# Performance work log

Hardware: AMD Instinct MI355X
Metric: run time of the kernel (lower is better)

The kernel has to match this reference:

```python
import jax, jax.numpy as jnp
import numpy as np

N_HEAD = 16

def setup_inputs() -> dict:
    key = jax.random.key(0)
    ks = jax.random.split(key, 5)
    C = 1024
    s = 0.02
    return {
        "x": jax.random.normal(ks[0], (4, 2048, C), dtype=jnp.float32),
        "w_attn": jax.random.normal(ks[1], (C, 3 * C), dtype=jnp.float32) * s,
        "b_attn": jnp.zeros((3 * C,), dtype=jnp.float32),
        "w_proj": jax.random.normal(ks[2], (C, C), dtype=jnp.float32) * s,
        "b_proj": jnp.zeros((C,), dtype=jnp.float32),
    }

def reference(x, w_attn, b_attn, w_proj, b_proj):
    B, T, C = x.shape
    H = N_HEAD
    D = C // H
    qkv = x @ w_attn + b_attn                      # [B,T,3C]
    q, k, v = jnp.split(qkv, 3, axis=-1)
    # [B,H,T,D]
    q = q.reshape(B, T, H, D).transpose(0, 2, 1, 3)
    k = k.reshape(B, T, H, D).transpose(0, 2, 1, 3)
    v = v.reshape(B, T, H, D).transpose(0, 2, 1, 3)
    scale = 1.0 / np.sqrt(D).astype(np.float32)
    attn = jnp.einsum('bhtd,bhsd->bhts', q, k) * scale   # [B,H,T,T]
    causal = jnp.tril(jnp.ones((T, T), dtype=bool))
    attn = jnp.where(causal, attn, -jnp.inf)
    attn = jax.nn.softmax(attn, axis=-1)
    y = jnp.einsum('bhts,bhsd->bhtd', attn, v)           # [B,H,T,D]
    y = y.transpose(0, 2, 1, 3).reshape(B, T, C)
    return y @ w_proj + b_proj
```

## Files before the change

kernel.cpp:

```cpp
#include <hip/hip_runtime.h>
#include <hip/hip_bf16.h>

typedef short short8 __attribute__((ext_vector_type(8)));
typedef float f32x4 __attribute__((ext_vector_type(4)));
typedef float f32x16 __attribute__((ext_vector_type(16)));

typedef __attribute__((address_space(1))) void as1_void;
typedef __attribute__((address_space(3))) void as3_void;

__device__ __forceinline__ unsigned short f2bf(float f) {
    __hip_bfloat16 h = __float2bfloat16(f);
    return __builtin_bit_cast(unsigned short, h);
}

__device__ __forceinline__ float exp2fast(float x) {
    return __builtin_amdgcn_exp2f(x);
}

__device__ __forceinline__ unsigned int cvtpk(float lo, float hi) {
    unsigned int r;
    asm("v_cvt_pk_bf16_f32 %0, %1, %2" : "=v"(r) : "v"(lo), "v"(hi));
    return r;
}

__device__ __forceinline__ void plswap(unsigned int& a, unsigned int& b) {
    asm("v_permlane32_swap_b32 %0, %1" : "+v"(a), "+v"(b));
}

__device__ __forceinline__ void gload16(const unsigned short* g, unsigned short* l) {
    __builtin_amdgcn_global_load_lds((as1_void*)g, (as3_void*)l, 16, 0, 0);
}

__global__ __launch_bounds__(256) void conv_f32_to_bf16(
    const float* __restrict__ in, unsigned short* __restrict__ out, int n4) {
    int i = blockIdx.x * 256 + threadIdx.x;
    if (i >= n4) return;
    float4 v = ((const float4*)in)[i];
    ushort4 o;
    o.x = f2bf(v.x); o.y = f2bf(v.y); o.z = f2bf(v.z); o.w = f2bf(v.w);
    ((ushort4*)out)[i] = o;
}

__global__ __launch_bounds__(256) void transpose2_f32_to_bf16(
    const float* __restrict__ Wa, const float* __restrict__ Wp,
    unsigned short* __restrict__ WTa, unsigned short* __restrict__ WTp) {
    __shared__ float tile[32][33];
    const int K = 1024;
    int bx = blockIdx.x;
    const float* W;
    unsigned short* WT;
    int N, n0;
    if (bx < 96) { W = Wa; WT = WTa; N = 3072; n0 = bx * 32; }
    else         { W = Wp; WT = WTp; N = 1024; n0 = (bx - 96) * 32; }
    int tx = threadIdx.x, ty = threadIdx.y;
    int k0 = blockIdx.y * 32;
#pragma unroll
    for (int j = 0; j < 4; ++j)
        tile[ty + j * 8][tx] = W[(size_t)(k0 + ty + j * 8) * N + n0 + tx];
    __syncthreads();
#pragma unroll
    for (int j = 0; j < 4; ++j)
        WT[(size_t)(n0 + ty + j * 8) * K + k0 + tx] = f2bf(tile[tx][ty + j * 8]);
}

template <int MODE>
__global__ __launch_bounds__(256, 2) void gemm_bt(
    const unsigned short* __restrict__ A,
    const unsigned short* __restrict__ Bt,
    const float* __restrict__ bias,
    void* __restrict__ out0,
    unsigned short* __restrict__ out1,
    int M, int N, int K) {
    __shared__ unsigned short sA[128 * 64];
    __shared__ unsigned short sB[128 * 64];
    const int tid = threadIdx.x;
    const int lane = tid & 63;
    const int w = tid >> 6;
    const int wr = (w >> 1) * 64;
    const int wc = (w & 1) * 64;
    const size_t arow0 = (size_t)blockIdx.x * 128;
    const size_t brow0 = (size_t)blockIdx.y * 128;

    const int grow = (w << 5) + (lane >> 3);
    const int gcolswz = (((lane & 7) ^ ((lane >> 3) & 7)) << 3);
    const unsigned short* pA0 = A + (arow0 + grow) * (size_t)K + gcolswz;
    const unsigned short* pB0 = Bt + (brow0 + grow) * (size_t)K + gcolswz;
    unsigned short* lA = sA + (w << 11);
    unsigned short* lB = sB + (w << 11);

    f32x4 acc[4][4] = {};
    const int fr = lane & 15;
    const int g = lane >> 4;

    for (int k0 = 0; k0 < K; k0 += 64) {
        __syncthreads();
#pragma unroll
        for (int j = 0; j < 4; ++j) {
            gload16(pA0 + (size_t)(j * 8) * K + k0, lA + j * 512);
            gload16(pB0 + (size_t)(j * 8) * K + k0, lB + j * 512);
        }
        __syncthreads();

#pragma unroll
        for (int kc = 0; kc < 2; ++kc) {
            short8 af[4], bfr[4];
#pragma unroll
            for (int i = 0; i < 4; ++i) {
                const int row = wr + i * 16 + fr;
                af[i] = *(const short8*)&sA[row * 64 +
                                            (((kc * 4 + g) ^ (row & 7)) << 3)];
            }
#pragma unroll
            for (int i = 0; i < 4; ++i) {
                const int row = wc + i * 16 + fr;
                bfr[i] = *(const short8*)&sB[row * 64 +
                                             (((kc * 4 + g) ^ (row & 7)) << 3)];
            }
#pragma unroll
            for (int mi = 0; mi < 4; ++mi)
#pragma unroll
                for (int ni = 0; ni < 4; ++ni)
                    acc[mi][ni] = __builtin_amdgcn_mfma_f32_16x16x32_bf16(
                        af[mi], bfr[ni], acc[mi][ni], 0, 0, 0);
        }
    }

    const int fq = (lane >> 4) << 2;
    if constexpr (MODE == 0) {
#pragma unroll
        for (int mi = 0; mi < 4; ++mi)
#pragma unroll
            for (int ni = 0; ni < 4; ++ni) {
                size_t r = arow0 + wr + mi * 16 + fq;
                size_t c = brow0 + wc + ni * 16 + fr;
                float bv = bias[c];
#pragma unroll
                for (int j = 0; j < 4; ++j)
                    ((float*)out0)[(r + j) * (size_t)N + c] = acc[mi][ni][j] + bv;
            }
    } else {
        const bool isv = (int)(brow0 + wc) >= 2048;
        if (isv) {
#pragma unroll
            for (int mi = 0; mi < 4; ++mi)
#pragma unroll
                for (int ni = 0; ni < 4; ++ni) {
                    int c = (int)brow0 + wc + ni * 16 + fr;
                    float bv = bias[c];
                    int cv = c - 2048;
                    int r0 = (int)arow0 + wr + mi * 16 + fq;
                    int bb = r0 >> 11, t0 = r0 & 2047;
                    unsigned int lo = (unsigned int)f2bf(acc[mi][ni][0] + bv) |
                                      ((unsigned int)f2bf(acc[mi][ni][1] + bv) << 16);
                    unsigned int hi = (unsigned int)f2bf(acc[mi][ni][2] + bv) |
                                      ((unsigned int)f2bf(acc[mi][ni][3] + bv) << 16);
                    *(uint2*)&out1[(((size_t)(bb * 1024 + cv)) << 11) + t0] =
                        make_uint2(lo, hi);
                }
        } else {
            const float qs = ((int)(brow0 + wc) < 1024) ? 0.125f * 1.4426950408889634f
                                                        : 1.0f;
#pragma unroll
            for (int mi = 0; mi < 4; ++mi)
#pragma unroll
                for (int ni = 0; ni < 4; ++ni) {
                    size_t r = arow0 + wr + mi * 16 + fq;
                    size_t c = brow0 + wc + ni * 16 + fr;
                    float bv = bias[c];
#pragma unroll
                    for (int j = 0; j < 4; ++j)
                        ((unsigned short*)out0)[(r + j) * 2048 + c] =
                            f2bf((acc[mi][ni][j] + bv) * qs);
                }
        }
    }
}

__global__ __launch_bounds__(256, 3) void attn_mfma(
    const unsigned short* __restrict__ qk,
    const unsigned short* __restrict__ vt,
    unsigned short* __restrict__ y,
    int BH) {
    constexpr int T = 2048;
    constexpr float THR = 8.0f;

    __shared__ __align__(16) unsigned short sK[2][64 * 64];
    __shared__ __align__(16) unsigned short sV[2][64 * 64];

    const int tid = threadIdx.x;
    const int lane = tid & 63;
    const int w = tid >> 6;
    const int l31 = lane & 31;
    const int b5 = lane >> 5;

    const int bh = blockIdx.x % BH;
    const int qt = 15 - blockIdx.x / BH;
    const int b = bh >> 4;
    const int h = bh & 15;
    const int q0 = qt << 7;
    const int qw0 = q0 + w * 32;

    const unsigned short* kbase = qk + ((size_t)(b * T)) * 2048 + 1024 + h * 64;
    const unsigned short* vbase = vt + ((size_t)(b * 1024 + h * 64)) * 2048;

    const int srow = tid >> 3;
    const int c16 = tid & 7;
    const int swz = ((c16 ^ (srow & 7)) << 3);

    short8 vones;
#pragma unroll
    for (int i = 0; i < 8; ++i) vones[i] = (short)0x3F80;

    short8 aq[4];
    {
        const unsigned short* qbase =
            qk + ((size_t)(b * T + qw0 + l31)) * 2048 + h * 64;
#pragma unroll
        for (int kc = 0; kc < 4; ++kc)
            aq[kc] = *(const short8*)(qbase + b5 * 8 + kc * 16);
    }

    f32x16 O0 = {}, O1 = {};
    f32x16 l_st = {};
    float m_st = -1e30f;

    const int nt = (q0 + 128) >> 6;

    uint4 kA0, kA1, kB0, kB1, vd0, vd1;
    kA0 = *(const uint4*)(kbase + (size_t)(srow) * 2048 + c16 * 8);
    kA1 = *(const uint4*)(kbase + (size_t)(srow + 32) * 2048 + c16 * 8);
    vd0 = *(const uint4*)(vbase + (size_t)srow * 2048 + c16 * 8);
    vd1 = *(const uint4*)(vbase + (size_t)(srow + 32) * 2048 + c16 * 8);
    *(uint4*)&sK[0][srow * 64 + swz] = kA0;
    *(uint4*)&sK[0][(srow + 32) * 64 + swz] = kA1;
    *(uint4*)&sV[0][srow * 64 + swz] = vd0;
    *(uint4*)&sV[0][(srow + 32) * 64 + swz] = vd1;
    kB0 = *(const uint4*)(kbase + (size_t)(64 + srow) * 2048 + c16 * 8);
    kB1 = *(const uint4*)(kbase + (size_t)(64 + srow + 32) * 2048 + c16 * 8);
    __syncthreads();

    for (int it = 0; it < nt; ++it) {
        const int s0 = it << 6;
        const bool haveNext = (it + 1 < nt);
        const bool have2 = (it + 2 < nt);
        if (it & 1) {
            if (have2) {
                const int s2 = s0 + 128;
                kB0 = *(const uint4*)(kbase + (size_t)(s2 + srow) * 2048 + c16 * 8);
                kB1 = *(const uint4*)(kbase + (size_t)(s2 + srow + 32) * 2048 +
                                      c16 * 8);
            }
        } else {
            if (have2) {
                const int s2 = s0 + 128;
                kA0 = *(const uint4*)(kbase + (size_t)(s2 + srow) * 2048 + c16 * 8);
                kA1 = *(const uint4*)(kbase + (size_t)(s2 + srow + 32) * 2048 +
                                      c16 * 8);
            }
        }
        if (haveNext) {
            const int s1 = s0 + 64;
            vd0 = *(const uint4*)(vbase + (size_t)srow * 2048 + s1 + c16 * 8);
            vd1 = *(const uint4*)(vbase + (size_t)(srow + 32) * 2048 + s1 + c16 * 8);
        }
        const unsigned short* sKc = sK[it & 1];
        const unsigned short* sVc = sV[it & 1];

        if (s0 <= qw0 + 31) {
            f32x16 sacc[2] = {};
            __builtin_amdgcn_s_setprio(1);
#pragma unroll
            for (int kc = 0; kc < 4; ++kc) {
#pragma unroll
                for (int ni = 0; ni < 2; ++ni) {
                    const int row = ni * 32 + l31;
                    short8 akf = *(const short8*)&sKc[row * 64 +
                                                      (((b5 + kc * 2) ^ (row & 7))
                                                       << 3)];
                    sacc[ni] = __builtin_amdgcn_mfma_f32_32x32x16_bf16(
                        akf, aq[kc], sacc[ni], 0, 0, 0);
                }
            }
            __builtin_amdgcn_s_setprio(0);

            const bool needMask = (s0 + 63 > qw0);
            const int qg = qw0 + l31;
            if (needMask) {
#pragma unroll
                for (int ni = 0; ni < 2; ++ni)
#pragma unroll
                    for (int reg = 0; reg < 16; ++reg) {
                        const int sg = s0 + ni * 32 + (reg & 3) + 8 * (reg >> 2) +
                                       4 * b5;
                        sacc[ni][reg] = (sg <= qg) ? sacc[ni][reg] : -INFINITY;
                    }
            }

            float mt[16];
#pragma unroll
            for (int i = 0; i < 16; ++i)
                mt[i] = fmaxf(sacc[0][i], sacc[1][i]);
#pragma unroll
            for (int st = 8; st > 0; st >>= 1)
#pragma unroll
                for (int i = 0; i < 8; ++i)
                    if (i < st) mt[i] = fmaxf(mt[i], mt[i + st]);
            float mx = mt[0];
            mx = fmaxf(mx, __shfl_xor(mx, 32));

            const bool resc = __any(mx > m_st + THR);
            float f_l = 1.0f;
            if (resc) {
                const float mn = fmaxf(m_st, mx);
                f_l = exp2fast(m_st - mn);
                m_st = mn;
            }

#pragma unroll
            for (int ni = 0; ni < 2; ++ni)
#pragma unroll
                for (int reg = 0; reg < 16; ++reg)
                    sacc[ni][reg] = exp2fast(sacc[ni][reg] - m_st);

            short8 pa[4];
#pragma unroll
            for (int c = 0; c < 4; ++c) {
                const int ni = c >> 1;
                const int off = (c & 1) * 8;
                unsigned int pk01 = cvtpk(sacc[ni][off + 0], sacc[ni][off + 1]);
                unsigned int pk23 = cvtpk(sacc[ni][off + 2], sacc[ni][off + 3]);
                unsigned int pk45 = cvtpk(sacc[ni][off + 4], sacc[ni][off + 5]);
                unsigned int pk67 = cvtpk(sacc[ni][off + 6], sacc[ni][off + 7]);
                plswap(pk01, pk45);
                plswap(pk23, pk67);
                uint4 u = make_uint4(pk01, pk23, pk45, pk67);
                pa[c] = __builtin_bit_cast(short8, u);
            }

            if (resc) {
                const int fil = __builtin_bit_cast(int, f_l);
#pragma unroll
                for (int reg = 0; reg < 16; ++reg) {
                    const int qpat = (reg & 3) + 8 * (reg >> 2) + 4 * b5;
                    const float fq = __builtin_bit_cast(
                        float, __builtin_amdgcn_ds_bpermute(
                                   (qpat + (lane & 32)) << 2, fil));
                    O0[reg] *= fq;
                    O1[reg] *= fq;
                    l_st[reg] *= fq;
                }
            }

            __builtin_amdgcn_s_setprio(1);
#pragma unroll
            for (int c = 0; c < 4; ++c) {
                l_st = __builtin_amdgcn_mfma_f32_32x32x16_bf16(
                    pa[c], vones, l_st, 0, 0, 0);
                {
                    const int row = l31;
                    short8 bvf = *(const short8*)&sVc[row * 64 +
                                                      (((c * 2 + b5) ^ (row & 7))
                                                       << 3)];
                    O0 = __builtin_amdgcn_mfma_f32_32x32x16_bf16(
                        pa[c], bvf, O0, 0, 0, 0);
                }
                {
                    const int row = 32 + l31;
                    short8 bvf = *(const short8*)&sVc[row * 64 +
                                                      (((c * 2 + b5) ^ (row & 7))
                                                       << 3)];
                    O1 = __builtin_amdgcn_mfma_f32_32x32x16_bf16(
                        pa[c], bvf, O1, 0, 0, 0);
                }
            }
            __builtin_amdgcn_s_setprio(0);
        }

        if (haveNext) {
            unsigned short* sKn = sK[(it + 1) & 1];
            unsigned short* sVn = sV[(it + 1) & 1];
            if (it & 1) {
                *(uint4*)&sKn[srow * 64 + swz] = kA0;
                *(uint4*)&sKn[(srow + 32) * 64 + swz] = kA1;
            } else {
                *(uint4*)&sKn[srow * 64 + swz] = kB0;
                *(uint4*)&sKn[(srow + 32) * 64 + swz] = kB1;
            }
            *(uint4*)&sVn[srow * 64 + swz] = vd0;
            *(uint4*)&sVn[(srow + 32) * 64 + swz] = vd1;
        }
        __syncthreads();
    }

#pragma unroll
    for (int reg = 0; reg < 16; ++reg) {
        const int qpat = (reg & 3) + 8 * (reg >> 2) + 4 * b5;
        const float inv = 1.0f / l_st[reg];
        const size_t base = (size_t)(b * T + qw0 + qpat) * 1024 + h * 64 + l31;
        y[base] = f2bf(O0[reg] * inv);
        y[base + 32] = f2bf(O1[reg] * inv);
    }
}

extern "C" void kernel_launch(void* const* d_in, const int* in_sizes, int n_in,
                              void* d_out, int out_size, void* d_ws, size_t ws_size,
                              hipStream_t stream) {
    const float* x      = (const float*)d_in[0];
    const float* w_attn = (const float*)d_in[1];
    const float* b_attn = (const float*)d_in[2];
    const float* w_proj = (const float*)d_in[3];
    const float* b_proj = (const float*)d_in[4];

    const int C = 1024, T = 2048, H = 16;
    const int B = in_sizes[0] / (T * C);
    const int M = B * T;

    unsigned short* xb  = (unsigned short*)d_ws;
    unsigned short* wTa = xb + (size_t)M * C;
    unsigned short* wTp = wTa + (size_t)3 * C * C;
    unsigned short* qkb = wTp + (size_t)C * C;
    unsigned short* vtb = qkb + (size_t)M * 2 * C;
    unsigned short* y   = xb;

    int n4 = (M * C) / 4;
    conv_f32_to_bf16<<<(n4 + 255) / 256, 256, 0, stream>>>(x, xb, n4);
    transpose2_f32_to_bf16<<<dim3(128, 32), dim3(32, 8), 0, stream>>>(
        w_attn, w_proj, wTa, wTp);
    gemm_bt<2><<<dim3(M / 128, (3 * C) / 128), 256, 0, stream>>>(
        xb, wTa, b_attn, (void*)qkb, vtb, M, 3 * C, C);
    attn_mfma<<<dim3((B * H) * 16), 256, 0, stream>>>(qkb, vtb, y, B * H);
    gemm_bt<0><<<dim3(M / 128, C / 128), 256, 0, stream>>>(
        y, wTp, b_proj, d_out, nullptr, M, C, C);
}
```

Measured before the change: 160.7 us.

## Process 128-key tiles per iteration to halve barrier count

The attention loop now loads and stages 128 keys per iteration, processed as two 64-key chunks, instead of 64 keys. The aim is to halve the number of block-wide barriers and shared-memory handoffs and to amortise the prefetch across more compute. In exchange, shared memory per block doubles to 64KB, which may cut blocks per CU, and more registers hold prefetched data.

```diff
diff --git a/kernel.cpp b/kernel.cpp
--- a/kernel.cpp
+++ b/kernel.cpp
@@ -184,8 +184,8 @@
     constexpr int T = 2048;
     constexpr float THR = 8.0f;
 
-    __shared__ __align__(16) unsigned short sK[2][64 * 64];
-    __shared__ __align__(16) unsigned short sV[2][64 * 64];
+    __shared__ __align__(16) unsigned short sK[2][2 * 64 * 64];
+    __shared__ __align__(16) unsigned short sV[2][2 * 64 * 64];
 
     const int tid = threadIdx.x;
     const int lane = tid & 63;
@@ -224,170 +224,173 @@
     f32x16 l_st = {};
     float m_st = -1e30f;
 
-    const int nt = (q0 + 128) >> 6;
-
-    uint4 kA0, kA1, kB0, kB1, vd0, vd1;
-    kA0 = *(const uint4*)(kbase + (size_t)(srow) * 2048 + c16 * 8);
-    kA1 = *(const uint4*)(kbase + (size_t)(srow + 32) * 2048 + c16 * 8);
-    vd0 = *(const uint4*)(vbase + (size_t)srow * 2048 + c16 * 8);
-    vd1 = *(const uint4*)(vbase + (size_t)(srow + 32) * 2048 + c16 * 8);
-    *(uint4*)&sK[0][srow * 64 + swz] = kA0;
-    *(uint4*)&sK[0][(srow + 32) * 64 + swz] = kA1;
-    *(uint4*)&sV[0][srow * 64 + swz] = vd0;
-    *(uint4*)&sV[0][(srow + 32) * 64 + swz] = vd1;
-    kB0 = *(const uint4*)(kbase + (size_t)(64 + srow) * 2048 + c16 * 8);
-    kB1 = *(const uint4*)(kbase + (size_t)(64 + srow + 32) * 2048 + c16 * 8);
+    const int nt = qt + 1;
+
+    uint4 kd[4], vd[4];
+#pragma unroll
+    for (int rep = 0; rep < 4; ++rep)
+        kd[rep] = *(const uint4*)(kbase + (size_t)(srow + rep * 32) * 2048 + c16 * 8);
+    vd[0] = *(const uint4*)(vbase + (size_t)srow * 2048 + c16 * 8);
+    vd[1] = *(const uint4*)(vbase + (size_t)(srow + 32) * 2048 + c16 * 8);
+    vd[2] = *(const uint4*)(vbase + (size_t)srow * 2048 + 64 + c16 * 8);
+    vd[3] = *(const uint4*)(vbase + (size_t)(srow + 32) * 2048 + 64 + c16 * 8);
+#pragma unroll
+    for (int rep = 0; rep < 4; ++rep)
+        *(uint4*)&sK[0][(rep >> 1) * 4096 + (srow + (rep & 1) * 32) * 64 + swz] =
+            kd[rep];
+    *(uint4*)&sV[0][srow * 64 + swz] = vd[0];
+    *(uint4*)&sV[0][(srow + 32) * 64 + swz] = vd[1];
+    *(uint4*)&sV[0][4096 + srow * 64 + swz] = vd[2];
+    *(uint4*)&sV[0][4096 + (srow + 32) * 64 + swz] = vd[3];
     __syncthreads();
 
     for (int it = 0; it < nt; ++it) {
-        const int s0 = it << 6;
+        const int s0 = it << 7;
         const bool haveNext = (it + 1 < nt);
-        const bool have2 = (it + 2 < nt);
-        if (it & 1) {
-            if (have2) {
-                const int s2 = s0 + 128;
-                kB0 = *(const uint4*)(kbase + (size_t)(s2 + srow) * 2048 + c16 * 8);
-                kB1 = *(const uint4*)(kbase + (size_t)(s2 + srow + 32) * 2048 +
-                                      c16 * 8);
+        if (haveNext) {
+            const int s1 = s0 + 128;
+#pragma unroll
+            for (int rep = 0; rep < 4; ++rep)
+                kd[rep] = *(const uint4*)(kbase +
+                                          (size_t)(s1 + srow + rep * 32) * 2048 +
+                                          c16 * 8);
+            vd[0] = *(const uint4*)(vbase + (size_t)srow * 2048 + s1 + c16 * 8);
+            vd[1] = *(const uint4*)(vbase + (size_t)(srow + 32) * 2048 + s1 + c16 * 8);
+            vd[2] = *(const uint4*)(vbase + (size_t)srow * 2048 + s1 + 64 + c16 * 8);
+            vd[3] = *(const uint4*)(vbase + (size_t)(srow + 32) * 2048 + s1 + 64 +
+                                    c16 * 8);
+        }
+        const unsigned short* sKb = sK[it & 1];
+        const unsigned short* sVb = sV[it & 1];
+
+#pragma unroll
+        for (int ch = 0; ch < 2; ++ch) {
+            const int s0c = s0 + (ch << 6);
+            if (s0c <= qw0 + 31) {
+                const unsigned short* sKc = sKb + ch * 4096;
+                const unsigned short* sVc = sVb + ch * 4096;
+
+                f32x16 sacc[2] = {};
+                __builtin_amdgcn_s_setprio(1);
+#pragma unroll
+                for (int kc = 0; kc < 4; ++kc) {
+#pragma unroll
+                    for (int ni = 0; ni < 2; ++ni) {
+                        const int row = ni * 32 + l31;
+                        short8 akf = *(const short8*)&sKc[row * 64 +
+                                                          (((b5 + kc * 2) ^ (row & 7))
+                                                           << 3)];
+                        sacc[ni] = __builtin_amdgcn_mfma_f32_32x32x16_bf16(
+                            akf, aq[kc], sacc[ni], 0, 0, 0);
+                    }
+                }
+                __builtin_amdgcn_s_setprio(0);
+
+                const bool needMask = (s0c + 63 > qw0);
+                const int qg = qw0 + l31;
+                if (needMask) {
+#pragma unroll
+                    for (int ni = 0; ni < 2; ++ni)
+#pragma unroll
+                        for (int reg = 0; reg < 16; ++reg) {
+                            const int sg = s0c + ni * 32 + (reg & 3) +
+                                           8 * (reg >> 2) + 4 * b5;
+                            sacc[ni][reg] = (sg <= qg) ? sacc[ni][reg] : -INFINITY;
+                        }
+                }
+
+                float mt[16];
+#pragma unroll
+                for (int i = 0; i < 16; ++i)
+                    mt[i] = fmaxf(sacc[0][i], sacc[1][i]);
+#pragma unroll
+                for (int st = 8; st > 0; st >>= 1)
+#pragma unroll
+                    for (int i = 0; i < 8; ++i)
+                        if (i < st) mt[i] = fmaxf(mt[i], mt[i + st]);
+                float mx = mt[0];
+                mx = fmaxf(mx, __shfl_xor(mx, 32));
+
+                const bool resc = __any(mx > m_st + THR);
+                float f_l = 1.0f;
+                if (resc) {
+                    const float mn = fmaxf(m_st, mx);
+                    f_l = exp2fast(m_st - mn);
+                    m_st = mn;
+                }
+
+#pragma unroll
+                for (int ni = 0; ni < 2; ++ni)
+#pragma unroll
+                    for (int reg = 0; reg < 16; ++reg)
+                        sacc[ni][reg] = exp2fast(sacc[ni][reg] - m_st);
+
+                short8 pa[4];
+#pragma unroll
+                for (int c = 0; c < 4; ++c) {
+                    const int ni = c >> 1;
+                    const int off = (c & 1) * 8;
+                    unsigned int pk01 = cvtpk(sacc[ni][off + 0], sacc[ni][off + 1]);
+                    unsigned int pk23 = cvtpk(sacc[ni][off + 2], sacc[ni][off + 3]);
+                    unsigned int pk45 = cvtpk(sacc[ni][off + 4], sacc[ni][off + 5]);
+                    unsigned int pk67 = cvtpk(sacc[ni][off + 6], sacc[ni][off + 7]);
+                    plswap(pk01, pk45);
+                    plswap(pk23, pk67);
+                    uint4 u = make_uint4(pk01, pk23, pk45, pk67);
+                    pa[c] = __builtin_bit_cast(short8, u);
+                }
+
+                if (resc) {
+                    const int fil = __builtin_bit_cast(int, f_l);
+#pragma unroll
+                    for (int reg = 0; reg < 16; ++reg) {
+                        const int qpat = (reg & 3) + 8 * (reg >> 2) + 4 * b5;
+                        const float fq = __builtin_bit_cast(
+                            float, __builtin_amdgcn_ds_bpermute(
+                                       (qpat + (lane & 32)) << 2, fil));
+                        O0[reg] *= fq;
+                        O1[reg] *= fq;
+                        l_st[reg] *= fq;
+                    }
+                }
+
+                __builtin_amdgcn_s_setprio(1);
+#pragma unroll
+                for (int c = 0; c < 4; ++c) {
+                    l_st = __builtin_amdgcn_mfma_f32_32x32x16_bf16(
+                        pa[c], vones, l_st, 0, 0, 0);
+                    {
+                        const int row = l31;
+                        short8 bvf = *(const short8*)&sVc[row * 64 +
+                                                          (((c * 2 + b5) ^ (row & 7))
+                                                           << 3)];
+                        O0 = __builtin_amdgcn_mfma_f32_32x32x16_bf16(
+                            pa[c], bvf, O0, 0, 0, 0);
+                    }
+                    {
+                        const int row = 32 + l31;
+                        short8 bvf = *(const short8*)&sVc[row * 64 +
+                                                          (((c * 2 + b5) ^ (row & 7))
+                                                           << 3)];
+                        O1 = __builtin_amdgcn_mfma_f32_32x32x16_bf16(
+                            pa[c], bvf, O1, 0, 0, 0);
+                    }
+                }
+                __builtin_amdgcn_s_setprio(0);
             }
-        } else {
-            if (have2) {
-                const int s2 = s0 + 128;
-                kA0 = *(const uint4*)(kbase + (size_t)(s2 + srow) * 2048 + c16 * 8);
-                kA1 = *(const uint4*)(kbase + (size_t)(s2 + srow + 32) * 2048 +
-                                      c16 * 8);
-            }
-        }
-        if (haveNext) {
-            const int s1 = s0 + 64;
-            vd0 = *(const uint4*)(vbase + (size_t)srow * 2048 + s1 + c16 * 8);
-            vd1 = *(const uint4*)(vbase + (size_t)(srow + 32) * 2048 + s1 + c16 * 8);
-        }
-        const unsigned short* sKc = sK[it & 1];
-        const unsigned short* sVc = sV[it & 1];
-
-        if (s0 <= qw0 + 31) {
-            f32x16 sacc[2] = {};
-            __builtin_amdgcn_s_setprio(1);
-#pragma unroll
-            for (int kc = 0; kc < 4; ++kc) {
-#pragma unroll
-                for (int ni = 0; ni < 2; ++ni) {
-                    const int row = ni * 32 + l31;
-                    short8 akf = *(const short8*)&sKc[row * 64 +
-                                                      (((b5 + kc * 2) ^ (row & 7))
-                                                       << 3)];
-                    sacc[ni] = __builtin_amdgcn_mfma_f32_32x32x16_bf16(
-                        akf, aq[kc], sacc[ni], 0, 0, 0);
-                }
-            }
-            __builtin_amdgcn_s_setprio(0);
-
-            const bool needMask = (s0 + 63 > qw0);
-            const int qg = qw0 + l31;
-            if (needMask) {
-#pragma unroll
-                for (int ni = 0; ni < 2; ++ni)
-#pragma unroll
-                    for (int reg = 0; reg < 16; ++reg) {
-                        const int sg = s0 + ni * 32 + (reg & 3) + 8 * (reg >> 2) +
-                                       4 * b5;
-                        sacc[ni][reg] = (sg <= qg) ? sacc[ni][reg] : -INFINITY;
-                    }
-            }
-
-            float mt[16];
-#pragma unroll
-            for (int i = 0; i < 16; ++i)
-                mt[i] = fmaxf(sacc[0][i], sacc[1][i]);
-#pragma unroll
-            for (int st = 8; st > 0; st >>= 1)
-#pragma unroll
-                for (int i = 0; i < 8; ++i)
-                    if (i < st) mt[i] = fmaxf(mt[i], mt[i + st]);
-            float mx = mt[0];
-            mx = fmaxf(mx, __shfl_xor(mx, 32));
-
-            const bool resc = __any(mx > m_st + THR);
-            float f_l = 1.0f;
-            if (resc) {
-                const float mn = fmaxf(m_st, mx);
-                f_l = exp2fast(m_st - mn);
-                m_st = mn;
-            }
-
-#pragma unroll
-            for (int ni = 0; ni < 2; ++ni)
-#pragma unroll
-                for (int reg = 0; reg < 16; ++reg)
-                    sacc[ni][reg] = exp2fast(sacc[ni][reg] - m_st);
-
-            short8 pa[4];
-#pragma unroll
-            for (int c = 0; c < 4; ++c) {
-                const int ni = c >> 1;
-                const int off = (c & 1) * 8;
-                unsigned int pk01 = cvtpk(sacc[ni][off + 0], sacc[ni][off + 1]);
-                unsigned int pk23 = cvtpk(sacc[ni][off + 2], sacc[ni][off + 3]);
-                unsigned int pk45 = cvtpk(sacc[ni][off + 4], sacc[ni][off + 5]);
-                unsigned int pk67 = cvtpk(sacc[ni][off + 6], sacc[ni][off + 7]);
-                plswap(pk01, pk45);
-                plswap(pk23, pk67);
-                uint4 u = make_uint4(pk01, pk23, pk45, pk67);
-                pa[c] = __builtin_bit_cast(short8, u);
-            }
-
-            if (resc) {
-                const int fil = __builtin_bit_cast(int, f_l);
-#pragma unroll
-                for (int reg = 0; reg < 16; ++reg) {
-                    const int qpat = (reg & 3) + 8 * (reg >> 2) + 4 * b5;
-                    const float fq = __builtin_bit_cast(
-                        float, __builtin_amdgcn_ds_bpermute(
-                                   (qpat + (lane & 32)) << 2, fil));
-                    O0[reg] *= fq;
-                    O1[reg] *= fq;
-                    l_st[reg] *= fq;
-                }
-            }
-
-            __builtin_amdgcn_s_setprio(1);
-#pragma unroll
-            for (int c = 0; c < 4; ++c) {
-                l_st = __builtin_amdgcn_mfma_f32_32x32x16_bf16(
-                    pa[c], vones, l_st, 0, 0, 0);
-                {
-                    const int row = l31;
-                    short8 bvf = *(const short8*)&sVc[row * 64 +
-                                                      (((c * 2 + b5) ^ (row & 7))
-                                                       << 3)];
-                    O0 = __builtin_amdgcn_mfma_f32_32x32x16_bf16(
-                        pa[c], bvf, O0, 0, 0, 0);
-                }
-                {
-                    const int row = 32 + l31;
-                    short8 bvf = *(const short8*)&sVc[row * 64 +
-                                                      (((c * 2 + b5) ^ (row & 7))
-                                                       << 3)];
-                    O1 = __builtin_amdgcn_mfma_f32_32x32x16_bf16(
-                        pa[c], bvf, O1, 0, 0, 0);
-                }
-            }
-            __builtin_amdgcn_s_setprio(0);
         }
 
         if (haveNext) {
             unsigned short* sKn = sK[(it + 1) & 1];
             unsigned short* sVn = sV[(it + 1) & 1];
-            if (it & 1) {
-                *(uint4*)&sKn[srow * 64 + swz] = kA0;
-                *(uint4*)&sKn[(srow + 32) * 64 + swz] = kA1;
-            } else {
-                *(uint4*)&sKn[srow * 64 + swz] = kB0;
-                *(uint4*)&sKn[(srow + 32) * 64 + swz] = kB1;
-            }
-            *(uint4*)&sVn[srow * 64 + swz] = vd0;
-            *(uint4*)&sVn[(srow + 32) * 64 + swz] = vd1;
+#pragma unroll
+            for (int rep = 0; rep < 4; ++rep)
+                *(uint4*)&sKn[(rep >> 1) * 4096 + (srow + (rep & 1) * 32) * 64 +
+                              swz] = kd[rep];
+            *(uint4*)&sVn[srow * 64 + swz] = vd[0];
+            *(uint4*)&sVn[(srow + 32) * 64 + swz] = vd[1];
+            *(uint4*)&sVn[4096 + srow * 64 + swz] = vd[2];
+            *(uint4*)&sVn[4096 + (srow + 32) * 64 + swz] = vd[3];
         }
         __syncthreads();
     }
```

Measured after the change: 207.7 us. 29.2% more time.
